# Kernel optimization log

Hardware: AMD Instinct MI355X
Metric: run time of the kernel (lower is better)

Reference implementation:

```python
import jax, jax.numpy as jnp
import numpy as np

DIM = 512
HEADS = 8
DIM_HEAD = 64
INNER = HEADS * DIM_HEAD  # 512
B, N = 4, 2048


def setup_inputs() -> dict:
    key = jax.random.key(0)
    k1, k2, k3, k4 = jax.random.split(key, 4)
    x = jax.random.normal(k1, (B, N, DIM), dtype=jnp.float32)
    # nn.Linear(dim, inner*3, bias=False): weight [3*inner, dim]; store transposed [dim, 3*inner]
    w_qkv = jax.random.normal(k2, (DIM, 3 * INNER), dtype=jnp.float32) / np.sqrt(DIM)
    w_out = jax.random.normal(k3, (INNER, DIM), dtype=jnp.float32) / np.sqrt(INNER)
    b_out = jax.random.normal(k4, (DIM,), dtype=jnp.float32) * 0.01
    return {"x": x, "w_qkv": w_qkv, "w_out": w_out, "b_out": b_out}


def reference(x, w_qkv, w_out, b_out):
    b, n, _ = x.shape
    scale = DIM_HEAD ** -0.5
    qkv = x @ w_qkv  # [b, n, 3*inner]
    q, k, v = jnp.split(qkv, 3, axis=-1)
    # [b, n, h, d] -> [b, h, n, d]
    reshape = lambda t: t.reshape(b, n, HEADS, DIM_HEAD).transpose(0, 2, 1, 3)
    q, k, v = reshape(q), reshape(k), reshape(v)
    dots = jnp.einsum('bhid,bhjd->bhij', q, k) * scale  # [b, h, n, n]
    attn = jax.nn.softmax(dots, axis=-1)
    out = jnp.einsum('bhij,bhjd->bhid', attn, v)  # [b, h, n, d]
    out = out.transpose(0, 2, 1, 3).reshape(b, n, INNER)
    return out @ w_out + b_out  # dropout is identity at inference
```

## Files before the change

kernel.cpp:

```cpp
#include <hip/hip_runtime.h>
#include <hip/hip_bf16.h>
#include <cstdint>

#define DEV __device__ __forceinline__

typedef __attribute__((ext_vector_type(8))) __bf16 bf16x8;
typedef __attribute__((ext_vector_type(4))) float floatx4;
typedef __attribute__((ext_vector_type(4))) short shortx4;
typedef __attribute__((ext_vector_type(8))) short shortx8;

constexpr float QSCALE = 0.18033688011112042f;

DEV unsigned short f2b(float f) {
  union { float f; unsigned u; } v; v.f = f;
  return (unsigned short)((v.u + 0x7fffu + ((v.u >> 16) & 1u)) >> 16);
}

#if defined(__has_builtin) && __has_builtin(__builtin_amdgcn_cvt_pk_bf16_f32)
DEV unsigned pk2(float a, float b) {
  typedef __attribute__((ext_vector_type(2))) __bf16 bf2;
  union { bf2 v; unsigned u; } u;
  u.v = __builtin_amdgcn_cvt_pk_bf16_f32(a, b);
  return u.u;
}
#else
DEV unsigned pk2(float a, float b) {
  return (unsigned)f2b(a) | ((unsigned)f2b(b) << 16);
}
#endif

#if defined(__has_builtin) && __has_builtin(__builtin_amdgcn_exp2f)
DEV float fexp2(float x) { return __builtin_amdgcn_exp2f(x); }
#else
DEV float fexp2(float x) { return exp2f(x); }
#endif

DEV floatx4 mfma16(bf16x8 a, bf16x8 b, floatx4 c) {
  return __builtin_amdgcn_mfma_f32_16x16x32_bf16(a, b, c, 0, 0, 0);
}

#define GLD_LDS16(gp, lp)                                                          \
  __builtin_amdgcn_global_load_lds(                                                \
      (const __attribute__((address_space(1))) void*)(gp),                         \
      (__attribute__((address_space(3))) void*)(lp), 16, 0, 0)

__global__ void cvt_f32_bf16(const float* __restrict__ in,
                             unsigned short* __restrict__ out, int n4) {
  int i = blockIdx.x * 256 + threadIdx.x;
  if (i >= n4) return;
  floatx4 f = ((const floatx4*)in)[i];
  shortx4 s;
  s[0] = (short)f2b(f[0]); s[1] = (short)f2b(f[1]);
  s[2] = (short)f2b(f[2]); s[3] = (short)f2b(f[3]);
  ((shortx4*)out)[i] = s;
}

__global__ void tcvt2(const float* __restrict__ w_qkv,
                      const float* __restrict__ w_out,
                      unsigned short* __restrict__ wqkvt,
                      unsigned short* __restrict__ woutt) {
  __shared__ float tile[32][33];
  const float* in; unsigned short* out; int C, bx;
  if (blockIdx.x < 48) { in = w_qkv; out = wqkvt; C = 1536; bx = blockIdx.x; }
  else { in = w_out; out = woutt; C = 512; bx = blockIdx.x - 48; }
  const int R = 512;
  int tx = threadIdx.x & 31, ty = threadIdx.x >> 5;
  int r0 = blockIdx.y * 32, c0 = bx * 32;
#pragma unroll
  for (int i = 0; i < 4; i++) {
    int rr = ty + i * 8;
    tile[rr][tx] = in[(size_t)(r0 + rr) * C + c0 + tx];
  }
  __syncthreads();
#pragma unroll
  for (int i = 0; i < 4; i++) {
    int rr = ty + i * 8;
    out[(size_t)(c0 + rr) * R + r0 + tx] = f2b(tile[tx][rr]);
  }
}

__global__ __launch_bounds__(256, 3) void gemm_qkv(
    const unsigned short* __restrict__ A, const unsigned short* __restrict__ Bt,
    unsigned short* __restrict__ qf, unsigned short* __restrict__ kg,
    unsigned short* __restrict__ vf) {
  __shared__ __align__(16) unsigned short smem[17408];
  const int tid = threadIdx.x;
  const int lane = tid & 63, wid = tid >> 6;
  const int g = lane >> 4, r = lane & 15;
  const int m0 = blockIdx.y * 128, n0 = blockIdx.x * 128;
  const int wm = (wid & 1) * 64, wn = (wid >> 1) * 64;
  const int K = 512;

  floatx4 acc[4][4] = {};

  int rowA[2], kbA[2];
#pragma unroll
  for (int i = 0; i < 2; i++) {
    int c = i * 256 + tid;
    rowA[i] = c >> 2;
    kbA[i] = (c & 3) ^ ((rowA[i] >> 1) & 3);
  }

#define STAGE_G(kt, b)                                                           \
  {                                                                              \
    _Pragma("unroll") for (int i = 0; i < 2; i++) {                              \
      GLD_LDS16(A + (size_t)(m0 + rowA[i]) * K + (kt) + kbA[i] * 8,              \
                (char*)smem + (b)*8192 + i * 4096 + wid * 1024);                 \
      GLD_LDS16(Bt + (size_t)(n0 + rowA[i]) * K + (kt) + kbA[i] * 8,             \
                (char*)smem + 16384 + (b)*8192 + i * 4096 + wid * 1024);         \
    }                                                                            \
  }

  STAGE_G(0, 0)
  for (int it = 0; it < 16; it++) {
    const int buf = it & 1;
    __syncthreads();
    if (it + 1 < 16) STAGE_G((it + 1) * 32, buf ^ 1)
    const unsigned short* Xs = smem + buf * 4096;
    const unsigned short* Ws = smem + 8192 + buf * 4096;
    bf16x8 a[4], b[4];
#pragma unroll
    for (int t = 0; t < 4; t++) {
      int rw = wm + t * 16 + r;
      a[t] = *(const bf16x8*)(Xs + rw * 32 + (g ^ ((rw >> 1) & 3)) * 8);
      int rb = wn + t * 16 + r;
      b[t] = *(const bf16x8*)(Ws + rb * 32 + (g ^ ((rb >> 1) & 3)) * 8);
    }
#pragma unroll
    for (int mt = 0; mt < 4; mt++)
#pragma unroll
      for (int nt = 0; nt < 4; nt++)
        acc[mt][nt] = mfma16(a[mt], b[nt], acc[mt][nt]);
  }
#undef STAGE_G

  const int which = blockIdx.x >> 2;
  if (which == 2) {
    const int tokbase = m0 + wm;
    const int bb = tokbase >> 11, vt = (tokbase & 2047) >> 6;
#pragma unroll
    for (int nt = 0; nt < 4; nt++) {
      int vcol = n0 + wn + nt * 16 + r - 1024;
      int h = vcol >> 6;
      size_t hb = (size_t)(bb * 8 + h) * 131072 + (size_t)vt * 4096 + nt * 1024 +
                  (g * 16 + r) * 8;
#pragma unroll
      for (int kc = 0; kc < 2; kc++) {
        union { unsigned u[4]; shortx8 v; } w;
        w.u[0] = pk2(acc[2 * kc][nt][0], acc[2 * kc][nt][1]);
        w.u[1] = pk2(acc[2 * kc][nt][2], acc[2 * kc][nt][3]);
        w.u[2] = pk2(acc[2 * kc + 1][nt][0], acc[2 * kc + 1][nt][1]);
        w.u[3] = pk2(acc[2 * kc + 1][nt][2], acc[2 * kc + 1][nt][3]);
        *(shortx8*)(vf + hb + kc * 512) = w.v;
      }
    }
  } else {
    const float sc = (which == 0) ? QSCALE : 1.f;
    __syncthreads();
#pragma unroll
    for (int mt = 0; mt < 4; mt++)
#pragma unroll
      for (int nt = 0; nt < 4; nt++) {
        int col = wn + nt * 16 + r;
#pragma unroll
        for (int e = 0; e < 4; e++)
          smem[(wm + mt * 16 + g * 4 + e) * 136 + col] = f2b(acc[mt][nt][e] * sc);
      }
    __syncthreads();
#pragma unroll
    for (int it = 0; it < 8; it++) {
      int c = it * 256 + tid;
      int row = c >> 4, cc = c & 15;
      shortx8 v = *(const shortx8*)(smem + row * 136 + cc * 8);
      int gq = n0 + cc * 8;
      int h = (gq >> 6) & 7, d0 = gq & 63;
      int tok = m0 + row, bb = tok >> 11, n = tok & 2047;
      if (which == 0) {
        int kc = d0 >> 5, gp = (d0 >> 3) & 3;
        *(shortx8*)(qf + (size_t)(bb * 8 + h) * 131072 + (n >> 4) * 1024 +
                    kc * 512 + (gp * 16 + (n & 15)) * 8) = v;
      } else {
        *(shortx8*)(kg + ((size_t)(bb * 8 + h) * 2048 + n) * 64 + d0) = v;
      }
    }
  }
}

__global__ __launch_bounds__(256, 2) void gemm_out(
    const unsigned short* __restrict__ A, const unsigned short* __restrict__ Bt,
    float* __restrict__ outF, const float* __restrict__ bias) {
  __shared__ __align__(16) unsigned short smem[16896];
  const int tid = threadIdx.x;
  const int lane = tid & 63, wid = tid >> 6;
  const int g = lane >> 4, r = lane & 15;
  const int m0 = blockIdx.y * 64, n0 = blockIdx.x * 128;
  const int wn = wid * 32;
  const int K = 512;

  floatx4 acc[4][2] = {};

  const int rA = tid >> 2, kA = (tid & 3) ^ ((rA >> 1) & 3);
  int rB[2], kB[2];
#pragma unroll
  for (int i = 0; i < 2; i++) {
    int c = i * 256 + tid;
    rB[i] = c >> 2;
    kB[i] = (c & 3) ^ ((rB[i] >> 1) & 3);
  }

#define STAGE_O(kt, b)                                                           \
  {                                                                              \
    GLD_LDS16(A + (size_t)(m0 + rA) * K + (kt) + kA * 8,                         \
              (char*)smem + (b)*4096 + wid * 1024);                              \
    _Pragma("unroll") for (int i = 0; i < 2; i++)                                \
        GLD_LDS16(Bt + (size_t)(n0 + rB[i]) * K + (kt) + kB[i] * 8,              \
                  (char*)smem + 8192 + (b)*8192 + i * 4096 + wid * 1024);        \
  }

  STAGE_O(0, 0)
  for (int it = 0; it < 16; it++) {
    const int buf = it & 1;
    __syncthreads();
    if (it + 1 < 16) STAGE_O((it + 1) * 32, buf ^ 1)
    const unsigned short* Xs = smem + buf * 2048;
    const unsigned short* Ws = smem + 4096 + buf * 4096;
    bf16x8 a[4], b[2];
#pragma unroll
    for (int t = 0; t < 4; t++) {
      int rw = t * 16 + r;
      a[t] = *(const bf16x8*)(Xs + rw * 32 + (g ^ ((rw >> 1) & 3)) * 8);
    }
#pragma unroll
    for (int t = 0; t < 2; t++) {
      int rb = wn + t * 16 + r;
      b[t] = *(const bf16x8*)(Ws + rb * 32 + (g ^ ((rb >> 1) & 3)) * 8);
    }
#pragma unroll
    for (int mt = 0; mt < 4; mt++)
#pragma unroll
      for (int bt = 0; bt < 2; bt++)
        acc[mt][bt] = mfma16(a[mt], b[bt], acc[mt][bt]);
  }
#undef STAGE_O

  float* ftile = (float*)smem;
  __syncthreads();
#pragma unroll
  for (int mt = 0; mt < 4; mt++)
#pragma unroll
    for (int bt = 0; bt < 2; bt++)
#pragma unroll
      for (int e = 0; e < 4; e++)
        ftile[(mt * 16 + g * 4 + e) * 132 + wn + bt * 16 + r] = acc[mt][bt][e];
  __syncthreads();
#pragma unroll
  for (int it = 0; it < 8; it++) {
    int c = it * 256 + tid;
    int lr = c >> 5, cc = c & 31;
    floatx4 v = *(const floatx4*)(ftile + lr * 132 + cc * 4);
    int col = n0 + cc * 4;
    v += *(const floatx4*)(bias + col);
    *(floatx4*)(outF + (size_t)(m0 + lr) * 512 + col) = v;
  }
}

__global__ __launch_bounds__(256, 4) void attn(
    const unsigned short* __restrict__ qf, const unsigned short* __restrict__ kg,
    const unsigned short* __restrict__ vf, unsigned short* __restrict__ ao) {
  __shared__ __align__(16) char L[32768];
  unsigned short* Ksm = (unsigned short*)L;
  const int tid = threadIdx.x, lane = tid & 63, wid = tid >> 6;
  const int g = lane >> 4, r = lane & 15, r7 = r & 7;
  const int wq = wid & 1, wk = wid >> 1;
  const int slot = blockIdx.x;
  const int bh = ((slot & 7) << 2) | ((slot >> 3) & 3);
  const int qt = slot >> 5;
  const size_t kbase = (size_t)bh * (2048 * 64);
  const size_t fbase = (size_t)bh * 131072;
  const unsigned short* vb = vf + fbase;
  const int srow = lane >> 3;
  const int chunk = (lane & 7) ^ (srow & 7);

  const int qt0 = qt * 4 + wq * 2;
  bf16x8 bq[2][2];
#pragma unroll
  for (int nt = 0; nt < 2; nt++)
#pragma unroll
    for (int kc = 0; kc < 2; kc++)
      bq[nt][kc] = *(const bf16x8*)(qf + fbase + (size_t)(qt0 + nt) * 1024 +
                                    kc * 512 + lane * 8);

  bf16x8 vones;
#pragma unroll
  for (int i = 0; i < 8; i++) vones[i] = (__bf16)1.0f;

  floatx4 o[2][4] = {};
  floatx4 lacc[2] = {};

#define STAGE_K(rnd, b)                                                          \
  {                                                                              \
    _Pragma("unroll") for (int j = 0; j < 4; j++) {                              \
      int row = (rnd)*128 + wid * 32 + j * 8 + srow;                             \
      GLD_LDS16(kg + kbase + (size_t)row * 64 + chunk * 8,                       \
                (char*)L + (b)*16384 + wid * 4096 + j * 1024);                   \
    }                                                                            \
  }

  STAGE_K(0, 0)
  for (int rnd = 0; rnd < 16; rnd++) {
    const int buf = rnd & 1;
    __syncthreads();
    if (rnd + 1 < 16) STAGE_K(rnd + 1, buf ^ 1)
    const unsigned short* Ks_ = Ksm + buf * 8192 + wk * 64 * 64;
    const int vt = rnd * 2 + wk;

    floatx4 st[4][2] = {};
    __builtin_amdgcn_s_setprio(1);
#pragma unroll
    for (int kc = 0; kc < 2; kc++)
#pragma unroll
      for (int mt = 0; mt < 4; mt++) {
        bf16x8 ak = *(const bf16x8*)(Ks_ + (mt * 16 + r) * 64 +
                                     ((kc * 4 + g) ^ r7) * 8);
#pragma unroll
        for (int nt = 0; nt < 2; nt++)
          st[mt][nt] = mfma16(ak, bq[nt][kc], st[mt][nt]);
      }
    __builtin_amdgcn_s_setprio(0);

    bf16x8 ap[2][2];
#pragma unroll
    for (int a = 0; a < 2; a++) {
      float p[4][4];
#pragma unroll
      for (int mt = 0; mt < 4; mt++)
#pragma unroll
        for (int e = 0; e < 4; e++) p[mt][e] = fexp2(st[mt][a][e]);
#pragma unroll
      for (int kc = 0; kc < 2; kc++) {
        union { unsigned u[4]; bf16x8 v; } w;
        w.u[0] = pk2(p[2 * kc][0], p[2 * kc][1]);
        w.u[1] = pk2(p[2 * kc][2], p[2 * kc][3]);
        w.u[2] = pk2(p[2 * kc + 1][0], p[2 * kc + 1][1]);
        w.u[3] = pk2(p[2 * kc + 1][2], p[2 * kc + 1][3]);
        ap[a][kc] = w.v;
      }
    }

    bf16x8 bv[4][2];
#pragma unroll
    for (int b = 0; b < 4; b++)
#pragma unroll
      for (int kc = 0; kc < 2; kc++)
        bv[b][kc] = *(const bf16x8*)(vb + (size_t)vt * 4096 + b * 1024 +
                                     kc * 512 + lane * 8);

    __builtin_amdgcn_s_setprio(1);
#pragma unroll
    for (int kc = 0; kc < 2; kc++)
#pragma unroll
      for (int a = 0; a < 2; a++) {
        lacc[a] = mfma16(ap[a][kc], vones, lacc[a]);
#pragma unroll
        for (int b = 0; b < 4; b++)
          o[a][b] = mfma16(ap[a][kc], bv[b][kc], o[a][b]);
      }
    __builtin_amdgcn_s_setprio(0);
  }
#undef STAGE_K

  float* fP = (float*)L;
  float* fL = (float*)(L + 16384);
  unsigned short* Osm = (unsigned short*)(L + 20480);
  __syncthreads();
  if (wk == 1) {
#pragma unroll
    for (int a = 0; a < 2; a++) {
      *(floatx4*)&fL[wq * 512 + a * 256 + lane * 4] = lacc[a];
#pragma unroll
      for (int b = 0; b < 4; b++)
        *(floatx4*)&fP[wq * 2048 + (a * 4 + b) * 256 + lane * 4] = o[a][b];
    }
  }
  __syncthreads();
  if (wk == 0) {
#pragma unroll
    for (int a = 0; a < 2; a++) {
      floatx4 lt = lacc[a] + *(floatx4*)&fL[wq * 512 + a * 256 + lane * 4];
      floatx4 il;
#pragma unroll
      for (int e = 0; e < 4; e++) il[e] = 1.f / lt[e];
#pragma unroll
      for (int b = 0; b < 4; b++) {
        floatx4 oo = o[a][b] +
                     *(floatx4*)&fP[wq * 2048 + (a * 4 + b) * 256 + lane * 4];
#pragma unroll
        for (int e = 0; e < 4; e++)
          Osm[wq * 2304 + (a * 16 + g * 4 + e) * 72 + b * 16 + r] =
              f2b(oo[e] * il[e]);
      }
    }
  }
  __syncthreads();
  const int bb = bh >> 3, h = bh & 7;
#pragma unroll
  for (int it = 0; it < 2; it++) {
    int c = it * 256 + tid;
    int row = c >> 3, cc = c & 7;
    int wqi = row >> 5, r5 = row & 31;
    shortx8 v = *(const shortx8*)(Osm + wqi * 2304 + r5 * 72 + cc * 8);
    int tok = qt * 64 + row;
    *(shortx8*)(ao + ((size_t)(bb * 2048 + tok)) * 512 + h * 64 + cc * 8) = v;
  }
}

extern "C" void kernel_launch(void* const* d_in, const int* in_sizes, int n_in,
                              void* d_out, int out_size, void* d_ws, size_t ws_size,
                              hipStream_t stream) {
  const float* x = (const float*)d_in[0];
  const float* w_qkv = (const float*)d_in[1];
  const float* w_out = (const float*)d_in[2];
  const float* b_out = (const float*)d_in[3];
  float* out = (float*)d_out;

  unsigned short* wsp = (unsigned short*)d_ws;
  unsigned short* xb = wsp;
  unsigned short* wqkvt = xb + (size_t)8192 * 512;
  unsigned short* woutt = wqkvt + (size_t)1536 * 512;
  unsigned short* qf = woutt + (size_t)512 * 512;
  unsigned short* kg = qf + (size_t)32 * 2048 * 64;
  unsigned short* vf = kg + (size_t)32 * 2048 * 64;
  unsigned short* ao = vf + (size_t)32 * 2048 * 64;

  cvt_f32_bf16<<<4096, 256, 0, stream>>>(x, xb, 8192 * 512 / 4);
  tcvt2<<<dim3(64, 16), 256, 0, stream>>>(w_qkv, w_out, wqkvt, woutt);
  gemm_qkv<<<dim3(12, 64), 256, 0, stream>>>(xb, wqkvt, qf, kg, vf);
  attn<<<dim3(1024), 256, 0, stream>>>(qf, kg, vf, ao);
  gemm_out<<<dim3(4, 128), 256, 0, stream>>>(ao, woutt, out, b_out);
}
```

Baseline: 155.6 us.

## Merge prep kernels, hoist V loads, and restructure attention QK loop

The separate x conversion and weight transpose kernels become one launch, which removes one kernel launch and its gap. In the attention kernel the V fragment loads move ahead of the QK^T MFMAs so their global latency overlaps compute. Pointer arithmetic is replaced with incrementing pointers, and the QK accumulation chain is restructured per mt. Launch bounds drop from 4 to 3 waves per SIMD, trading occupancy for register headroom, which may hurt latency hiding.

```diff
diff --git a/kernel.cpp b/kernel.cpp
--- a/kernel.cpp
+++ b/kernel.cpp
@@ -44,28 +44,30 @@
       (const __attribute__((address_space(1))) void*)(gp),                         \
       (__attribute__((address_space(3))) void*)(lp), 16, 0, 0)
 
-__global__ void cvt_f32_bf16(const float* __restrict__ in,
-                             unsigned short* __restrict__ out, int n4) {
-  int i = blockIdx.x * 256 + threadIdx.x;
-  if (i >= n4) return;
-  floatx4 f = ((const floatx4*)in)[i];
-  shortx4 s;
-  s[0] = (short)f2b(f[0]); s[1] = (short)f2b(f[1]);
-  s[2] = (short)f2b(f[2]); s[3] = (short)f2b(f[3]);
-  ((shortx4*)out)[i] = s;
-}
-
-__global__ void tcvt2(const float* __restrict__ w_qkv,
-                      const float* __restrict__ w_out,
-                      unsigned short* __restrict__ wqkvt,
-                      unsigned short* __restrict__ woutt) {
+__global__ void prep(const float* __restrict__ x,
+                     const float* __restrict__ w_qkv,
+                     const float* __restrict__ w_out,
+                     unsigned short* __restrict__ xb,
+                     unsigned short* __restrict__ wqkvt,
+                     unsigned short* __restrict__ woutt) {
   __shared__ float tile[32][33];
+  if (blockIdx.x < 4096) {
+    int i = blockIdx.x * 256 + threadIdx.x;
+    floatx4 f = ((const floatx4*)x)[i];
+    shortx4 s;
+    s[0] = (short)f2b(f[0]); s[1] = (short)f2b(f[1]);
+    s[2] = (short)f2b(f[2]); s[3] = (short)f2b(f[3]);
+    ((shortx4*)xb)[i] = s;
+    return;
+  }
+  int id = blockIdx.x - 4096;
+  int bxr = id & 63, by = id >> 6;
   const float* in; unsigned short* out; int C, bx;
-  if (blockIdx.x < 48) { in = w_qkv; out = wqkvt; C = 1536; bx = blockIdx.x; }
-  else { in = w_out; out = woutt; C = 512; bx = blockIdx.x - 48; }
+  if (bxr < 48) { in = w_qkv; out = wqkvt; C = 1536; bx = bxr; }
+  else { in = w_out; out = woutt; C = 512; bx = bxr - 48; }
   const int R = 512;
   int tx = threadIdx.x & 31, ty = threadIdx.x >> 5;
-  int r0 = blockIdx.y * 32, c0 = bx * 32;
+  int r0 = by * 32, c0 = bx * 32;
 #pragma unroll
   for (int i = 0; i < 4; i++) {
     int rr = ty + i * 8;
@@ -264,20 +266,19 @@
   }
 }
 
-__global__ __launch_bounds__(256, 4) void attn(
+__global__ __launch_bounds__(256, 3) void attn(
     const unsigned short* __restrict__ qf, const unsigned short* __restrict__ kg,
     const unsigned short* __restrict__ vf, unsigned short* __restrict__ ao) {
   __shared__ __align__(16) char L[32768];
   unsigned short* Ksm = (unsigned short*)L;
   const int tid = threadIdx.x, lane = tid & 63, wid = tid >> 6;
-  const int g = lane >> 4, r = lane & 15, r7 = r & 7;
+  const int g = lane >> 4, r = lane & 15, r7 = r & 15 & 7;
   const int wq = wid & 1, wk = wid >> 1;
   const int slot = blockIdx.x;
   const int bh = ((slot & 7) << 2) | ((slot >> 3) & 3);
   const int qt = slot >> 5;
   const size_t kbase = (size_t)bh * (2048 * 64);
   const size_t fbase = (size_t)bh * 131072;
-  const unsigned short* vb = vf + fbase;
   const int srow = lane >> 3;
   const int chunk = (lane & 7) ^ (srow & 7);
 
@@ -293,39 +294,49 @@
   bf16x8 vones;
 #pragma unroll
   for (int i = 0; i < 8; i++) vones[i] = (__bf16)1.0f;
+  const floatx4 fzero = {0.f, 0.f, 0.f, 0.f};
 
   floatx4 o[2][4] = {};
   floatx4 lacc[2] = {};
 
-#define STAGE_K(rnd, b)                                                          \
+  const unsigned short* vbp = vf + fbase + (size_t)wk * 4096 + lane * 8;
+  const unsigned short* kgp =
+      kg + kbase + (size_t)(wid * 32 + srow) * 64 + chunk * 8;
+
+#define STAGE_K(b)                                                               \
   {                                                                              \
     _Pragma("unroll") for (int j = 0; j < 4; j++) {                              \
-      int row = (rnd)*128 + wid * 32 + j * 8 + srow;                             \
-      GLD_LDS16(kg + kbase + (size_t)row * 64 + chunk * 8,                       \
-                (char*)L + (b)*16384 + wid * 4096 + j * 1024);                   \
+      GLD_LDS16(kgp + j * 512, (char*)L + (b)*16384 + wid * 4096 + j * 1024);    \
     }                                                                            \
-  }
-
-  STAGE_K(0, 0)
+    kgp += 8192;                                                                 \
+  }
+
+  STAGE_K(0)
   for (int rnd = 0; rnd < 16; rnd++) {
     const int buf = rnd & 1;
     __syncthreads();
-    if (rnd + 1 < 16) STAGE_K(rnd + 1, buf ^ 1)
-    const unsigned short* Ks_ = Ksm + buf * 8192 + wk * 64 * 64;
-    const int vt = rnd * 2 + wk;
-
-    floatx4 st[4][2] = {};
+    if (rnd + 1 < 16) STAGE_K(buf ^ 1)
+    const unsigned short* Ks_ = Ksm + buf * 8192 + wk * 4096;
+
+    bf16x8 bv[4][2];
+#pragma unroll
+    for (int b = 0; b < 4; b++)
+#pragma unroll
+      for (int kc = 0; kc < 2; kc++)
+        bv[b][kc] = *(const bf16x8*)(vbp + b * 1024 + kc * 512);
+
+    floatx4 st[4][2];
     __builtin_amdgcn_s_setprio(1);
 #pragma unroll
-    for (int kc = 0; kc < 2; kc++)
-#pragma unroll
-      for (int mt = 0; mt < 4; mt++) {
-        bf16x8 ak = *(const bf16x8*)(Ks_ + (mt * 16 + r) * 64 +
-                                     ((kc * 4 + g) ^ r7) * 8);
-#pragma unroll
-        for (int nt = 0; nt < 2; nt++)
-          st[mt][nt] = mfma16(ak, bq[nt][kc], st[mt][nt]);
-      }
+    for (int mt = 0; mt < 4; mt++) {
+      bf16x8 ak0 = *(const bf16x8*)(Ks_ + (mt * 16 + r) * 64 + (g ^ r7) * 8);
+      bf16x8 ak1 = *(const bf16x8*)(Ks_ + (mt * 16 + r) * 64 + ((4 + g) ^ r7) * 8);
+#pragma unroll
+      for (int nt = 0; nt < 2; nt++) {
+        floatx4 t = mfma16(ak0, bq[nt][0], fzero);
+        st[mt][nt] = mfma16(ak1, bq[nt][1], t);
+      }
+    }
     __builtin_amdgcn_s_setprio(0);
 
     bf16x8 ap[2][2];
@@ -347,14 +358,6 @@
       }
     }
 
-    bf16x8 bv[4][2];
-#pragma unroll
-    for (int b = 0; b < 4; b++)
-#pragma unroll
-      for (int kc = 0; kc < 2; kc++)
-        bv[b][kc] = *(const bf16x8*)(vb + (size_t)vt * 4096 + b * 1024 +
-                                     kc * 512 + lane * 8);
-
     __builtin_amdgcn_s_setprio(1);
 #pragma unroll
     for (int kc = 0; kc < 2; kc++)
@@ -366,6 +369,7 @@
           o[a][b] = mfma16(ap[a][kc], bv[b][kc], o[a][b]);
       }
     __builtin_amdgcn_s_setprio(0);
+    vbp += 8192;
   }
 #undef STAGE_K
 
@@ -432,8 +436,7 @@
   unsigned short* vf = kg + (size_t)32 * 2048 * 64;
   unsigned short* ao = vf + (size_t)32 * 2048 * 64;
 
-  cvt_f32_bf16<<<4096, 256, 0, stream>>>(x, xb, 8192 * 512 / 4);
-  tcvt2<<<dim3(64, 16), 256, 0, stream>>>(w_qkv, w_out, wqkvt, woutt);
+  prep<<<5120, 256, 0, stream>>>(x, w_qkv, w_out, xb, wqkvt, woutt);
   gemm_qkv<<<dim3(12, 64), 256, 0, stream>>>(xb, wqkvt, qf, kg, vf);
   attn<<<dim3(1024), 256, 0, stream>>>(qf, kg, vf, ao);
   gemm_out<<<dim3(4, 128), 256, 0, stream>>>(ao, woutt, out, b_out);
```

New measurement: 153.9 us. Within noise of the previous version (-1.1%).
